# Kernel optimization log

Measured on AMD Instinct MI355X. Metric: run time of the kernel, lower is better.

## Reference

```python
import jax, jax.numpy as jnp
import numpy as np

B, DIN, D = 1000, 1024, 512
C, L = 1203, 77
N_INS, N_EX = 4, 5
K_SEL, K_TOP = 32, 5
HEADS, DH, MLP, NL = 8, 64, 2048, 4
TEMP = 50.0


def setup_inputs() -> dict:
    key = jax.random.key(0)
    ks = iter(jax.random.split(key, 64))

    def rn(shape, s=0.02):
        return jax.random.normal(next(ks), shape, dtype=jnp.float32) * s

    def layer_params(prefix):
        return {
            prefix + '_ln1_g': jnp.ones((NL, D)), prefix + '_ln1_b': jnp.zeros((NL, D)),
            prefix + '_qkv_w': rn((NL, D, 3 * D)), prefix + '_qkv_b': jnp.zeros((NL, 3 * D)),
            prefix + '_out_w': rn((NL, D, D)), prefix + '_out_b': jnp.zeros((NL, D)),
            prefix + '_ln2_g': jnp.ones((NL, D)), prefix + '_ln2_b': jnp.zeros((NL, D)),
            prefix + '_fc_w': rn((NL, D, MLP)), prefix + '_fc_b': jnp.zeros((NL, MLP)),
            prefix + '_pr_w': rn((NL, MLP, D)), prefix + '_pr_b': jnp.zeros((NL, D)),
        }

    zw = jax.random.normal(next(ks), (D, C + 1), dtype=jnp.float32)
    zw = zw / jnp.linalg.norm(zw, axis=0, keepdims=True)  # F.normalize(dim=0) as in __init__
    inp = {
        'x': jax.random.normal(next(ks), (B, DIN), dtype=jnp.float32),
        'linear_w': rn((DIN, D)), 'linear_b': jnp.zeros((D,)),
        'zs_weight': zw,
        'sample_w': rn((D, D)), 'sample_b': jnp.zeros((D,)),
        'ins_token': rn((N_INS, D), 0.1),
        'token_seq': rn((C, L, D), 0.1),
        'exemplar': rn((C, N_EX, D), 0.1),
        'eos_index': jax.random.randint(next(ks), (C,), 5, 60, dtype=jnp.int32),
    }
    inp.update(layer_params('agg'))
    inp['pos_emb'] = rn((L, D), 0.01)
    inp.update(layer_params('txt'))
    inp['lnf_g'] = jnp.ones((D,))
    inp['lnf_b'] = jnp.zeros((D,))
    inp['text_proj'] = rn((D, D))
    return inp


def layernorm(x, g, b, eps=1e-5):
    m = x.mean(-1, keepdims=True)
    v = x.var(-1, keepdims=True)
    return (x - m) * jax.lax.rsqrt(v + eps) * g + b


def quick_gelu(x):  # CLIP QuickGELU
    return x * jax.nn.sigmoid(1.702 * x)


def transformer(h, ln1g, ln1b, qkvw, qkvb, ow, ob, ln2g, ln2b, fcw, fcb, prw, prb, mask=None):
    # h: [N, S, D]; pre-LN residual attention blocks (CLIP style)
    Bn, S, _ = h.shape
    scale = np.float32(1.0 / np.sqrt(DH))
    for i in range(NL):
        a = layernorm(h, ln1g[i], ln1b[i])
        qkv = a @ qkvw[i] + qkvb[i]
        q, k, v = jnp.split(qkv, 3, axis=-1)
        q = q.reshape(Bn, S, HEADS, DH)
        k = k.reshape(Bn, S, HEADS, DH)
        v = v.reshape(Bn, S, HEADS, DH)
        s = jnp.einsum('bqhd,bkhd->bhqk', q, k) * scale
        if mask is not None:
            s = s + mask
        o = jnp.einsum('bhqk,bkhd->bqhd', jax.nn.softmax(s, axis=-1), v).reshape(Bn, S, D)
        h = h + o @ ow[i] + ob[i]
        m = layernorm(h, ln2g[i], ln2b[i])
        h = h + quick_gelu(m @ fcw[i] + fcb[i]) @ prw[i] + prb[i]
    return h


def inverse_sigmoid(x, eps=1e-5):
    x = jnp.clip(x, 0.0, 1.0)
    x1 = jnp.clip(x, eps, None)
    x2 = jnp.clip(1.0 - x, eps, None)
    return jnp.log(x1 / x2)


def reference(x, linear_w, linear_b, zs_weight, sample_w, sample_b, ins_token, token_seq,
              exemplar, eos_index,
              agg_ln1_g, agg_ln1_b, agg_qkv_w, agg_qkv_b, agg_out_w, agg_out_b,
              agg_ln2_g, agg_ln2_b, agg_fc_w, agg_fc_b, agg_pr_w, agg_pr_b,
              pos_emb, txt_ln1_g, txt_ln1_b, txt_qkv_w, txt_qkv_b, txt_out_w, txt_out_b,
              txt_ln2_g, txt_ln2_b, txt_fc_w, txt_fc_b, txt_pr_w, txt_pr_b,
              lnf_g, lnf_b, text_proj):
    # ---- base classifier ----
    h = x @ linear_w + linear_b                                        # [B, D]
    h = TEMP * h / jnp.linalg.norm(h, axis=1, keepdims=True)
    logits = h @ zs_weight                                             # [B, C+1]
    # ---- entropy-based proposal selection (eval path, k=32) ----
    p = jax.nn.sigmoid(logits)
    entropy = (-p * jax.nn.log_sigmoid(logits)).sum(-1)                # [B]
    _, select_index = jax.lax.top_k(entropy, K_SEL)                    # [32]
    sel_logits = logits[select_index]                                  # [32, C+1]
    _, topk_index = jax.lax.top_k(sel_logits[:, :-1], K_TOP)           # [32, 5]
    sampled_x = jax.lax.stop_gradient(h[select_index]) @ sample_w + sample_b  # [32, D]
    # ---- batched aggregator input (replaces per-proposal python loop) ----
    base = ins_token[None] + (sampled_x / TEMP)[:, None, :]            # [32, N_INS, D]
    base = jnp.broadcast_to(base[:, None], (K_SEL, K_TOP, N_INS, D))
    ex = exemplar[topk_index]                                          # [32, 5, N_EX, D]
    agg_in = jnp.concatenate([base, ex], axis=2).reshape(K_SEL * K_TOP, N_INS + N_EX, D)
    agg_out = transformer(agg_in, agg_ln1_g, agg_ln1_b, agg_qkv_w, agg_qkv_b, agg_out_w,
                          agg_out_b, agg_ln2_g, agg_ln2_b, agg_fc_w, agg_fc_b, agg_pr_w, agg_pr_b)
    ins_tokens = agg_out[:, :N_INS].reshape(K_SEL, K_TOP, N_INS, D)
    # ---- splice instance tokens into class prompts ----
    prompt = token_seq[topk_index]                                     # [32, 5, L, D]
    upd = jnp.concatenate([prompt[:, :, :2], ins_tokens, prompt[:, :, 2:L - N_INS]], axis=2)
    # ---- CLIP text encoder on updated prompts ----
    t = upd.reshape(K_SEL * K_TOP, L, D) + pos_emb
    causal = jnp.where(jnp.tril(jnp.ones((L, L), bool)), 0.0, -1e9).astype(jnp.float32)
    t = transformer(t, txt_ln1_g, txt_ln1_b, txt_qkv_w, txt_qkv_b, txt_out_w, txt_out_b,
                    txt_ln2_g, txt_ln2_b, txt_fc_w, txt_fc_b, txt_pr_w, txt_pr_b, mask=causal)
    t = layernorm(t, lnf_g, lnf_b)
    eos = (eos_index[topk_index] + 2 * N_INS).reshape(-1)              # [160]
    feats = t[jnp.arange(K_SEL * K_TOP), eos] @ text_proj              # [160, D]
    feats = feats / jnp.linalg.norm(feats, axis=-1, keepdims=True)
    rerank_logits = jnp.einsum('sd,skd->sk', sampled_x, feats.reshape(K_SEL, K_TOP, D))
    # ---- fuse + scatter back ----
    sel_det = jax.lax.stop_gradient(sel_logits)
    sel_topk = jnp.take_along_axis(sel_det, topk_index, axis=1)
    fused = jax.nn.sigmoid(sel_topk) ** 0.75 * jax.nn.sigmoid(rerank_logits) ** 0.25
    reranked = inverse_sigmoid(fused)
    rows = jnp.arange(K_SEL)[:, None]
    logits_clone = sel_det.at[rows, topk_index].set(reranked)
    logits_final = logits.at[select_index].set(logits_clone)
    return logits, rerank_logits, select_index, logits_final
```

## Files before the change

### kernel.cpp

```cpp
#include <hip/hip_runtime.h>
#include <math.h>

#define TID ((int)threadIdx.x)

constexpr int Bsz = 1000, DIN = 1024, Dm = 512, C1 = 1204, C0 = 1203, Ltok = 77;
constexpr int NINS = 4, NEX = 5, KSEL = 32, KTOP = 5, NHEAD = 8, DH = 64, MLPD = 2048, NL = 4, Pn = 160;
constexpr float TEMPc = 50.0f;

typedef __attribute__((ext_vector_type(8))) short short8;
typedef __attribute__((ext_vector_type(4))) float f32x4;
typedef __attribute__((address_space(1))) const void g1void;
typedef __attribute__((address_space(3))) void l3void;
#define GLOAD16(g, l) __builtin_amdgcn_global_load_lds((g1void*)(g), (l3void*)(l), 16, 0, 0)

__device__ __forceinline__ float sigf(float z) {
  return z >= 0.f ? 1.f / (1.f + expf(-z)) : expf(z) / (1.f + expf(z));
}

__device__ __forceinline__ float qgelu(float v) {
  return v * __fdividef(1.f, 1.f + __expf(-1.702f * v));
}

__device__ __forceinline__ unsigned short f2bfu(float f) {
  unsigned u = __builtin_bit_cast(unsigned, f);
  u += 0x7fffu + ((u >> 16) & 1u);
  return (unsigned short)(u >> 16);
}
__device__ __forceinline__ short f2bf(float f) { return (short)f2bfu(f); }

__global__ __launch_bounds__(256, 4) void bgemm_k(const short* __restrict__ A,
                                                  const short* __restrict__ Bt,
                                                  const float* __restrict__ bias,
                                                  float* __restrict__ Cf,
                                                  short* __restrict__ Cb,
                                                  float* __restrict__ Xres,
                                                  int M, int N, int K, int mode) {
  __shared__ short As[8192];
  __shared__ short Bs[8192];
  int nwg = gridDim.x * gridDim.y;
  int orig = blockIdx.y * gridDim.x + blockIdx.x;
  int xcd = orig & 7, lid = orig >> 3;
  int q = nwg >> 3, r = nwg & 7;
  int swz = (xcd < r ? xcd * (q + 1) : r * (q + 1) + (xcd - r) * q) + lid;
  int row0 = (swz / gridDim.x) * 128, col0 = (swz % gridDim.x) * 128;
  int lane = TID & 63;
  int w = TID >> 6;
  int wr = (TID >> 7) & 1, wc = (TID >> 6) & 1;
  int skb = (TID >> 4) & 3, si = TID & 15;
  f32x4 acc[4][4] = {};
  int nt = K >> 6;
  int kb = lane >> 4, i = lane & 15;
  for (int t = 0; t < nt; ++t) {
#pragma unroll
    for (int s = 0; s < 2; ++s) {
#pragma unroll
      for (int c = 0; c < 2; ++c) {
        int row = (c * 4 + w) * 16 + si;
        int k0 = (t << 6) + (s << 5) + skb * 8;
        GLOAD16(A + (size_t)(row0 + row) * K + k0, As + s * 4096 + (c * 256 + w * 64) * 8);
        GLOAD16(Bt + (size_t)(col0 + row) * K + k0, Bs + s * 4096 + (c * 256 + w * 64) * 8);
      }
    }
    __syncthreads();
#pragma unroll
    for (int s = 0; s < 2; ++s) {
      const short* Ab = As + s * 4096;
      const short* Bb = Bs + s * 4096;
      short8 af[4], bfr[4];
#pragma unroll
      for (int m = 0; m < 4; ++m)
        af[m] = *(const short8*)(Ab + ((((wr * 4 + m) * 4 + kb) * 16 + i) * 8));
#pragma unroll
      for (int n = 0; n < 4; ++n)
        bfr[n] = *(const short8*)(Bb + ((((wc * 4 + n) * 4 + kb) * 16 + i) * 8));
#pragma unroll
      for (int m = 0; m < 4; ++m)
#pragma unroll
        for (int n = 0; n < 4; ++n)
          acc[m][n] = __builtin_amdgcn_mfma_f32_16x16x32_bf16(bfr[n], af[m], acc[m][n], 0, 0, 0);
    }
    __syncthreads();
  }
  int li = lane & 15, lg = lane >> 4;
#pragma unroll
  for (int m = 0; m < 4; ++m) {
    int row = row0 + wr * 64 + m * 16 + li;
    if (row >= M) continue;
#pragma unroll
    for (int n = 0; n < 4; ++n) {
      int colb = col0 + wc * 64 + n * 16 + lg * 4;
      f32x4 v = acc[m][n];
      if (bias) {
        float4 bv = *(const float4*)(bias + colb);
        v[0] += bv.x; v[1] += bv.y; v[2] += bv.z; v[3] += bv.w;
      }
      size_t off = (size_t)row * N + colb;
      if (mode == 0) {
        *(float4*)(Cf + off) = make_float4(v[0], v[1], v[2], v[3]);
      } else if (mode == 1) {
        float4* p = (float4*)(Xres + off);
        float4 o = *p;
        o.x += v[0]; o.y += v[1]; o.z += v[2]; o.w += v[3];
        *p = o;
      } else {
        if (mode == 2) {
          v[0] = qgelu(v[0]); v[1] = qgelu(v[1]); v[2] = qgelu(v[2]); v[3] = qgelu(v[3]);
        }
        uint2 pk;
        pk.x = (unsigned)f2bfu(v[0]) | ((unsigned)f2bfu(v[1]) << 16);
        pk.y = (unsigned)f2bfu(v[2]) | ((unsigned)f2bfu(v[3]) << 16);
        *(uint2*)(Cb + off) = pk;
      }
    }
  }
}

__global__ __launch_bounds__(256, 4) void bgemm_sk_k(const short* __restrict__ A,
                                                     const short* __restrict__ Bt,
                                                     float* __restrict__ P,
                                                     int M, int N, int K, int KC) {
  __shared__ short As[8192];
  __shared__ short Bs[8192];
  int nwg = gridDim.x * gridDim.y;
  int orig = blockIdx.y * gridDim.x + blockIdx.x;
  int xcd = orig & 7, lid = orig >> 3;
  int q = nwg >> 3, r = nwg & 7;
  int swz = (xcd < r ? xcd * (q + 1) : r * (q + 1) + (xcd - r) * q) + lid;
  int row0 = (swz / gridDim.x) * 128, col0 = (swz % gridDim.x) * 128;
  int kbeg = blockIdx.z * KC;
  int lane = TID & 63;
  int w = TID >> 6;
  int wr = (TID >> 7) & 1, wc = (TID >> 6) & 1;
  int skb = (TID >> 4) & 3, si = TID & 15;
  f32x4 acc[4][4] = {};
  int nt = KC >> 6;
  int kb = lane >> 4, i = lane & 15;
  for (int t = 0; t < nt; ++t) {
#pragma unroll
    for (int s = 0; s < 2; ++s) {
#pragma unroll
      for (int c = 0; c < 2; ++c) {
        int row = (c * 4 + w) * 16 + si;
        int k0 = kbeg + (t << 6) + (s << 5) + skb * 8;
        GLOAD16(A + (size_t)(row0 + row) * K + k0, As + s * 4096 + (c * 256 + w * 64) * 8);
        GLOAD16(Bt + (size_t)(col0 + row) * K + k0, Bs + s * 4096 + (c * 256 + w * 64) * 8);
      }
    }
    __syncthreads();
#pragma unroll
    for (int s = 0; s < 2; ++s) {
      const short* Ab = As + s * 4096;
      const short* Bb = Bs + s * 4096;
      short8 af[4], bfr[4];
#pragma unroll
      for (int m = 0; m < 4; ++m)
        af[m] = *(const short8*)(Ab + ((((wr * 4 + m) * 4 + kb) * 16 + i) * 8));
#pragma unroll
      for (int n = 0; n < 4; ++n)
        bfr[n] = *(const short8*)(Bb + ((((wc * 4 + n) * 4 + kb) * 16 + i) * 8));
#pragma unroll
      for (int m = 0; m < 4; ++m)
#pragma unroll
        for (int n = 0; n < 4; ++n)
          acc[m][n] = __builtin_amdgcn_mfma_f32_16x16x32_bf16(bfr[n], af[m], acc[m][n], 0, 0, 0);
    }
    __syncthreads();
  }
  float* Pz = P + (size_t)blockIdx.z * M * N;
  int li = lane & 15, lg = lane >> 4;
#pragma unroll
  for (int m = 0; m < 4; ++m) {
    int row = row0 + wr * 64 + m * 16 + li;
    if (row >= M) continue;
#pragma unroll
    for (int n = 0; n < 4; ++n) {
      int colb = col0 + wc * 64 + n * 16 + lg * 4;
      *(float4*)(Pz + (size_t)row * N + colb) = make_float4(acc[m][n][0], acc[m][n][1], acc[m][n][2], acc[m][n][3]);
    }
  }
}

__global__ __launch_bounds__(256) void reduce_res_k(const float* __restrict__ P,
                                                    const float* __restrict__ bias,
                                                    float* __restrict__ Xres,
                                                    int MN, int N, int S) {
  int i = blockIdx.x * 256 + TID;
  if (i >= MN) return;
  float v = bias[i % N];
  for (int s = 0; s < S; ++s) v += P[(size_t)s * MN + i];
  Xres[i] += v;
}

__global__ __launch_bounds__(256) void wconv_k(const float* __restrict__ W,
                                               short* __restrict__ Wt, int K, int N) {
  int l = blockIdx.z;
  const float* Wl = W + (size_t)l * K * N;
  short* Wtl = Wt + (size_t)l * K * N;
  __shared__ float t[32][33];
  int n0 = blockIdx.x * 32, k0 = blockIdx.y * 32;
  int tx = TID & 31, ty = TID >> 5;
#pragma unroll
  for (int u = 0; u < 4; ++u)
    t[ty + u * 8][tx] = Wl[(size_t)(k0 + ty + u * 8) * N + n0 + tx];
  __syncthreads();
#pragma unroll
  for (int u = 0; u < 4; ++u)
    Wtl[(size_t)(n0 + ty + u * 8) * K + k0 + tx] = f2bf(t[tx][ty + u * 8]);
}

__global__ __launch_bounds__(256) void gemm32s_k(const float* __restrict__ A,
                                                 const float* __restrict__ W,
                                                 float* __restrict__ P,
                                                 int M, int N, int K, int KC) {
  __shared__ float As[64][17];
  __shared__ float Ws[16][65];
  int tx = TID & 15, ty = TID >> 4;
  int row0 = blockIdx.y * 64, col0 = blockIdx.x * 64;
  int kbeg = blockIdx.z * KC;
  int kend = kbeg + KC < K ? kbeg + KC : K;
  float acc[4][4] = {};
  for (int k0 = kbeg; k0 < kend; k0 += 16) {
    {
      int r = TID >> 2, c4 = (TID & 3) * 4;
      int gr = row0 + r;
#pragma unroll
      for (int u = 0; u < 4; ++u) {
        int gc = k0 + c4 + u;
        As[r][c4 + u] = (gr < M && gc < K) ? A[gr * K + gc] : 0.f;
      }
    }
    {
      int c = TID & 63;
      int gc = col0 + c;
#pragma unroll
      for (int u = 0; u < 4; ++u) {
        int rr = (TID >> 6) * 4 + u;
        int gk = k0 + rr;
        Ws[rr][c] = (gk < K && gc < N) ? W[gk * N + gc] : 0.f;
      }
    }
    __syncthreads();
#pragma unroll
    for (int kk = 0; kk < 16; ++kk) {
      float a[4], b[4];
#pragma unroll
      for (int i = 0; i < 4; ++i) a[i] = As[ty * 4 + i][kk];
#pragma unroll
      for (int j = 0; j < 4; ++j) b[j] = Ws[kk][tx * 4 + j];
#pragma unroll
      for (int i = 0; i < 4; ++i)
#pragma unroll
        for (int j = 0; j < 4; ++j) acc[i][j] += a[i] * b[j];
    }
    __syncthreads();
  }
  float* Ps = P + (size_t)blockIdx.z * M * N;
#pragma unroll
  for (int i = 0; i < 4; ++i) {
    int rrow = row0 + ty * 4 + i;
    if (rrow >= M) continue;
#pragma unroll
    for (int j = 0; j < 4; ++j) {
      int ccol = col0 + tx * 4 + j;
      if (ccol >= N) continue;
      Ps[(size_t)rrow * N + ccol] = acc[i][j];
    }
  }
}

__global__ __launch_bounds__(256) void reduce_k(const float* __restrict__ P,
                                                const float* __restrict__ bias,
                                                float* __restrict__ C,
                                                float* __restrict__ C2,
                                                int MN, int N, int S) {
  int i = blockIdx.x * 256 + TID;
  if (i >= MN) return;
  float v = 0.f;
  for (int s = 0; s < S; ++s) v += P[(size_t)s * MN + i];
  if (bias) v += bias[i % N];
  C[i] = v;
  if (C2) C2[i] = v;
}

__global__ __launch_bounds__(256) void rownorm_k(float* __restrict__ h) {
  int r = blockIdx.x;
  float* x = h + r * Dm;
  float v0 = x[TID], v1 = x[TID + 256];
  __shared__ float s1[256];
  s1[TID] = v0 * v0 + v1 * v1;
  __syncthreads();
  for (int s = 128; s; s >>= 1) { if (TID < s) s1[TID] += s1[TID + s]; __syncthreads(); }
  float sc = TEMPc / sqrtf(s1[0]);
  x[TID] = v0 * sc;
  x[TID + 256] = v1 * sc;
}

__global__ __launch_bounds__(256) void entropy_k(const float* __restrict__ logits,
                                                 double* __restrict__ ent) {
  int r = blockIdx.x;
  double acc = 0.0;
  for (int c = TID; c < C1; c += 256) {
    float z = logits[r * C1 + c];
    float ls = z >= 0.f ? -log1pf(expf(-z)) : z - log1pf(expf(z));
    float p = z >= 0.f ? 1.f / (1.f + expf(-z)) : expf(z) / (1.f + expf(z));
    acc += (double)(-p * ls);
  }
  __shared__ double sd[256];
  sd[TID] = acc;
  __syncthreads();
  for (int s = 128; s; s >>= 1) { if (TID < s) sd[TID] += sd[TID + s]; __syncthreads(); }
  if (TID == 0) ent[r] = sd[0];
}

__global__ __launch_bounds__(256) void top32_k(const double* __restrict__ ent,
                                               int* __restrict__ selidx,
                                               float* __restrict__ out2) {
  __shared__ double v[1000];
  __shared__ double wv[4];
  __shared__ int wi[4];
  for (int i = TID; i < 1000; i += 256) v[i] = ent[i];
  __syncthreads();
  int w = TID >> 6, lane = TID & 63;
  for (int r = 0; r < KSEL; ++r) {
    double bv = -1e300; int bi = 1 << 30;
    for (int i = TID; i < 1000; i += 256) {
      double x = v[i];
      if (x > bv || (x == bv && i < bi)) { bv = x; bi = i; }
    }
#pragma unroll
    for (int off = 32; off; off >>= 1) {
      double ov = __shfl_xor(bv, off, 64);
      int oi = __shfl_xor(bi, off, 64);
      if (ov > bv || (ov == bv && oi < bi)) { bv = ov; bi = oi; }
    }
    if (lane == 0) { wv[w] = bv; wi[w] = bi; }
    __syncthreads();
    if (TID == 0) {
      double fv = wv[0]; int fi = wi[0];
#pragma unroll
      for (int u = 1; u < 4; ++u)
        if (wv[u] > fv || (wv[u] == fv && wi[u] < fi)) { fv = wv[u]; fi = wi[u]; }
      selidx[r] = fi; out2[r] = (float)fi; v[fi] = -1e300;
    }
    __syncthreads();
  }
}

__global__ __launch_bounds__(256) void top5_k(const float* __restrict__ logits,
                                              const int* __restrict__ selidx,
                                              int* __restrict__ topk) {
  int s = blockIdx.x;
  int row = selidx[s];
  __shared__ float v[C0];
  __shared__ float wv[4];
  __shared__ int wi[4];
  for (int i = TID; i < C0; i += 256) v[i] = logits[row * C1 + i];
  __syncthreads();
  int w = TID >> 6, lane = TID & 63;
  for (int r = 0; r < KTOP; ++r) {
    float bv = -INFINITY; int bi = 1 << 30;
    for (int i = TID; i < C0; i += 256) {
      float x = v[i];
      if (x > bv || (x == bv && i < bi)) { bv = x; bi = i; }
    }
#pragma unroll
    for (int off = 32; off; off >>= 1) {
      float ov = __shfl_xor(bv, off, 64);
      int oi = __shfl_xor(bi, off, 64);
      if (ov > bv || (ov == bv && oi < bi)) { bv = ov; bi = oi; }
    }
    if (lane == 0) { wv[w] = bv; wi[w] = bi; }
    __syncthreads();
    if (TID == 0) {
      float fv = wv[0]; int fi = wi[0];
#pragma unroll
      for (int u = 1; u < 4; ++u)
        if (wv[u] > fv || (wv[u] == fv && wi[u] < fi)) { fv = wv[u]; fi = wi[u]; }
      topk[s * KTOP + r] = fi; v[fi] = -INFINITY;
    }
    __syncthreads();
  }
}

__global__ void eos_k(const int* __restrict__ eos_index, const int* __restrict__ topk,
                      int* __restrict__ eosl) {
  for (int p = TID; p < Pn; p += 256) eosl[p] = eos_index[topk[p]] + 2 * NINS;
}

__global__ void gather_h_k(const float* __restrict__ h, const int* __restrict__ selidx,
                           float* __restrict__ hsel) {
  int s = blockIdx.x;
  int row = selidx[s];
  for (int d = TID; d < Dm; d += 256) hsel[s * Dm + d] = h[row * Dm + d];
}

__global__ __launch_bounds__(256) void build_agg_k(const float* __restrict__ ins,
                                                   const float* __restrict__ sampled,
                                                   const float* __restrict__ ex,
                                                   const int* __restrict__ topk,
                                                   float* __restrict__ X) {
  int b = blockIdx.x;
  int p = b / 9, tok = b % 9;
  int s = p / KTOP;
#pragma unroll
  for (int u = 0; u < 2; ++u) {
    int d = TID + u * 256;
    float v;
    if (tok < NINS) v = ins[tok * Dm + d] + sampled[s * Dm + d] * (1.f / TEMPc);
    else {
      int cls = topk[p];
      v = ex[(cls * NEX + (tok - NINS)) * Dm + d];
    }
    X[b * Dm + d] = v;
  }
}

__global__ void save_ins_k(const float* __restrict__ X, float* __restrict__ insbuf) {
  int p = blockIdx.x;
  for (int i = TID; i < NINS * Dm; i += 256) insbuf[p * NINS * Dm + i] = X[p * 9 * Dm + i];
}

__global__ __launch_bounds__(256) void build_txt_k(const float* __restrict__ token_seq,
                                                   const float* __restrict__ insbuf,
                                                   const float* __restrict__ pos,
                                                   const int* __restrict__ topk,
                                                   float* __restrict__ X, int p0) {
  int b = blockIdx.x;
  int pl = b / Ltok, tok = b % Ltok;
  int p = p0 + pl;
  int cls = topk[p];
#pragma unroll
  for (int u = 0; u < 2; ++u) {
    int d = TID + u * 256;
    float v;
    if (tok < 2) v = token_seq[(cls * Ltok + tok) * Dm + d];
    else if (tok < 2 + NINS) v = insbuf[(p * NINS + (tok - 2)) * Dm + d];
    else v = token_seq[(cls * Ltok + (tok - NINS)) * Dm + d];
    X[b * Dm + d] = v + pos[tok * Dm + d];
  }
}

__global__ __launch_bounds__(256) void ln_k(const float* __restrict__ X,
                                            const float* __restrict__ g,
                                            const float* __restrict__ b,
                                            short* __restrict__ A) {
  int t = blockIdx.x;
  const float* x = X + t * Dm;
  float v0 = x[TID], v1 = x[TID + 256];
  __shared__ float s1[256], s2[256];
  s1[TID] = v0 + v1;
  s2[TID] = v0 * v0 + v1 * v1;
  __syncthreads();
  for (int s = 128; s; s >>= 1) {
    if (TID < s) { s1[TID] += s1[TID + s]; s2[TID] += s2[TID + s]; }
    __syncthreads();
  }
  float mean = s1[0] * (1.f / 512.f);
  float var = s2[0] * (1.f / 512.f) - mean * mean;
  float inv = rsqrtf(var + 1e-5f);
  A[t * Dm + TID] = f2bf((v0 - mean) * inv * g[TID] + b[TID]);
  A[t * Dm + TID + 256] = f2bf((v1 - mean) * inv * g[TID + 256] + b[TID + 256]);
}

__global__ __launch_bounds__(320) void attn_tx_k(const short* __restrict__ qkv,
                                                 short* __restrict__ O, int S) {
  __shared__ short Kf[5120];
  __shared__ short Vt[6144];
  __shared__ short Pf[5][1536];
  int p = blockIdx.x >> 3, h = blockIdx.x & 7;
  int base = p * S;
  for (int c = TID; c < 640; c += 320) {
    int i = c & 15, kb = (c >> 4) & 7, g = c >> 7;
    int j = g * 16 + i;
    short8 v = {};
    if (j < S) v = *(const short8*)(qkv + (size_t)(base + j) * 1536 + 512 + h * 64 + kb * 8);
    *(short8*)(Kf + c * 8) = v;
  }
  for (int c = TID; c < 640; c += 320) {
    int j = c >> 3;
    int d0 = (c & 7) * 8;
    short8 v = {};
    if (j < S) v = *(const short8*)(qkv + (size_t)(base + j) * 1536 + 1024 + h * 64 + d0);
    int kb = j >> 3, jj = j & 7;
#pragma unroll
    for (int u = 0; u < 8; ++u) {
      int d = d0 + u;
      Vt[(((d >> 4) * 12 + kb) * 16 + (d & 15)) * 8 + jj] = v[u];
    }
  }
  for (int c = TID; c < 128; c += 320) {
    int i = c & 15, kb = 10 + ((c >> 4) & 1), g = c >> 5;
    *(short8*)(Vt + ((g * 12 + kb) * 16 + i) * 8) = short8{};
  }
  __syncthreads();
  int w = TID >> 6, lane = TID & 63;
  int li = lane & 15, lg = lane >> 4;
  short8 aq[2];
#pragma unroll
  for (int ks = 0; ks < 2; ++ks)
    aq[ks] = *(const short8*)(qkv + (size_t)(base + w * 16 + li) * 1536 + h * 64 + ks * 32 + lg * 8);
  f32x4 accs[5] = {};
#pragma unroll
  for (int t = 0; t < 5; ++t)
#pragma unroll
    for (int ks = 0; ks < 2; ++ks) {
      short8 bk = *(const short8*)(Kf + ((t * 8 + ks * 4 + lg) * 16 + li) * 8);
      accs[t] = __builtin_amdgcn_mfma_f32_16x16x32_bf16(aq[ks], bk, accs[t], 0, 0, 0);
    }
  int rowg = w * 16 + lg * 4;
#pragma unroll
  for (int r = 0; r < 4; ++r) {
    int row = rowg + r;
    float v[5];
    float mx = -1e30f;
#pragma unroll
    for (int t = 0; t < 5; ++t) {
      int col = t * 16 + li;
      float x = accs[t][r] * 0.125f;
      bool ok = (col < S) && (col <= row);
      v[t] = ok ? x : -1e30f;
      mx = fmaxf(mx, v[t]);
    }
#pragma unroll
    for (int off = 1; off < 16; off <<= 1) mx = fmaxf(mx, __shfl_xor(mx, off, 64));
    float sum = 0.f;
#pragma unroll
    for (int t = 0; t < 5; ++t) {
      v[t] = (v[t] > -1e29f) ? __expf(v[t] - mx) : 0.f;
      sum += v[t];
    }
#pragma unroll
    for (int off = 1; off < 16; off <<= 1) sum += __shfl_xor(sum, off, 64);
    float inv = __fdividef(1.f, sum);
#pragma unroll
    for (int t = 0; t < 5; ++t) {
      int c = t * 16 + li;
      Pf[w][((c >> 3) * 16 + (row - w * 16)) * 8 + (c & 7)] = f2bf(v[t] * inv);
    }
  }
  for (int z = lane; z < 256; z += 64) {
    int kb = 10 + (z >> 7);
    int rem = z & 127;
    Pf[w][(kb * 16 + (rem >> 3)) * 8 + (rem & 7)] = 0;
  }
  f32x4 acco[4] = {};
#pragma unroll
  for (int s = 0; s < 3; ++s) {
    short8 ap = *(const short8*)(Pf[w] + ((s * 4 + lg) * 16 + li) * 8);
#pragma unroll
    for (int n = 0; n < 4; ++n) {
      short8 bv = *(const short8*)(Vt + ((n * 12 + s * 4 + lg) * 16 + li) * 8);
      acco[n] = __builtin_amdgcn_mfma_f32_16x16x32_bf16(ap, bv, acco[n], 0, 0, 0);
    }
  }
#pragma unroll
  for (int n = 0; n < 4; ++n)
#pragma unroll
    for (int r = 0; r < 4; ++r) {
      int row = rowg + r;
      if (row < S) O[(size_t)(base + row) * 512 + h * 64 + n * 16 + li] = f2bf(acco[n][r]);
    }
}

__global__ __launch_bounds__(256) void attn_k(const float* __restrict__ qkv,
                                              short* __restrict__ O, int S, int causal) {
  int blk = blockIdx.x;
  int p = blk >> 3, h = blk & 7;
  __shared__ float Qs[Ltok][68], Ks[Ltok][68], Vs[Ltok][68];
  __shared__ float ps[4][132];
  int base = p * S;
  for (int idx = TID; idx < S * 16; idx += 256) {
    int j = idx >> 4, c = idx & 15;
    const float4* q = (const float4*)(qkv + (size_t)(base + j) * 1536 + h * 64);
    const float4* k = (const float4*)(qkv + (size_t)(base + j) * 1536 + 512 + h * 64);
    const float4* v = (const float4*)(qkv + (size_t)(base + j) * 1536 + 1024 + h * 64);
    ((float4*)&Qs[j][0])[c] = q[c];
    ((float4*)&Ks[j][0])[c] = k[c];
    ((float4*)&Vs[j][0])[c] = v[c];
  }
  __syncthreads();
  int wave = TID >> 6, lane = TID & 63;
  bool val0 = lane < S, val1 = lane + 64 < S;
  int j0 = val0 ? lane : 0;
  int j1 = val1 ? lane + 64 : 0;
  const float4* k0p = (const float4*)&Ks[j0][0];
  const float4* k1p = (const float4*)&Ks[j1][0];
  for (int i = wave; i < S; i += 4) {
    const float4* q4 = (const float4*)&Qs[i][0];
    float a0 = 0.f, a1 = 0.f;
#pragma unroll
    for (int d4 = 0; d4 < 16; ++d4) {
      float4 qv = q4[d4], k0v = k0p[d4], k1v = k1p[d4];
      a0 += qv.x * k0v.x + qv.y * k0v.y + qv.z * k0v.z + qv.w * k0v.w;
      a1 += qv.x * k1v.x + qv.y * k1v.y + qv.z * k1v.z + qv.w * k1v.w;
    }
    float m0 = (val0 && (!causal || lane <= i)) ? a0 * 0.125f : -1e30f;
    float m1 = (val1 && (!causal || lane + 64 <= i)) ? a1 * 0.125f : -1e30f;
    float mx = fmaxf(m0, m1);
#pragma unroll
    for (int off = 32; off; off >>= 1) mx = fmaxf(mx, __shfl_xor(mx, off, 64));
    float e0 = expf(m0 - mx), e1 = expf(m1 - mx);
    float sum = e0 + e1;
#pragma unroll
    for (int off = 32; off; off >>= 1) sum += __shfl_xor(sum, off, 64);
    float inv = 1.f / sum;
    ps[wave][lane] = e0 * inv;
    ps[wave][lane + 64] = e1 * inv;
    float o = 0.f;
    for (int j = 0; j < S; ++j) o += ps[wave][j] * Vs[j][lane];
    O[(base + i) * Dm + h * 64 + lane] = f2bf(o);
  }
}

__global__ __launch_bounds__(256) void feats_k(const float* __restrict__ X,
                                               const int* __restrict__ eosl,
                                               const float* __restrict__ g,
                                               const float* __restrict__ bb,
                                               const float* __restrict__ proj,
                                               float* __restrict__ feats, int p0) {
  int pl = blockIdx.x;
  int p = p0 + pl;
  int e = eosl[p];
  const float* x = X + (size_t)(pl * Ltok + e) * Dm;
  __shared__ float row[Dm];
  __shared__ float s1[256], s2[256];
  float v0 = x[TID], v1 = x[TID + 256];
  s1[TID] = v0 + v1;
  s2[TID] = v0 * v0 + v1 * v1;
  __syncthreads();
  for (int s = 128; s; s >>= 1) {
    if (TID < s) { s1[TID] += s1[TID + s]; s2[TID] += s2[TID + s]; }
    __syncthreads();
  }
  float mean = s1[0] * (1.f / 512.f);
  float var = s2[0] * (1.f / 512.f) - mean * mean;
  float inv = rsqrtf(var + 1e-5f);
  row[TID] = (v0 - mean) * inv * g[TID] + bb[TID];
  row[TID + 256] = (v1 - mean) * inv * g[TID + 256] + bb[TID + 256];
  __syncthreads();
  float a0 = 0.f, a1 = 0.f;
  for (int d = 0; d < Dm; ++d) {
    float r = row[d];
    a0 += r * proj[d * Dm + TID];
    a1 += r * proj[d * Dm + TID + 256];
  }
  s1[TID] = a0 * a0 + a1 * a1;
  __syncthreads();
  for (int s = 128; s; s >>= 1) { if (TID < s) s1[TID] += s1[TID + s]; __syncthreads(); }
  float sc = 1.f / sqrtf(s1[0]);
  feats[p * Dm + TID] = a0 * sc;
  feats[p * Dm + TID + 256] = a1 * sc;
}

__global__ void rerank_k(const float* __restrict__ sampled, const float* __restrict__ feats,
                         const int* __restrict__ selidx, const int* __restrict__ topk,
                         const float* __restrict__ logits, float* __restrict__ out1,
                         float* __restrict__ out3) {
  int idx = blockIdx.x;
  int s = idx / KTOP;
  int lane = TID;
  float acc = 0.f;
  for (int d = lane; d < Dm; d += 64) acc += sampled[s * Dm + d] * feats[idx * Dm + d];
#pragma unroll
  for (int off = 32; off; off >>= 1) acc += __shfl_down(acc, off, 64);
  if (lane == 0) {
    out1[idx] = acc;
    int row = selidx[s];
    int cls = topk[idx];
    float sl = logits[row * C1 + cls];
    float a = sigf(sl), b = sigf(acc);
    float fused = powf(a, 0.75f) * powf(b, 0.25f);
    float xx = fminf(fmaxf(fused, 0.f), 1.f);
    float x1 = fmaxf(xx, 1e-5f);
    float x2 = fmaxf(1.f - xx, 1e-5f);
    out3[row * C1 + cls] = logf(x1 / x2);
  }
}

static inline size_t alup(size_t x) { return (x + 255) & ~(size_t)255; }

constexpr size_t WT_QKV = (size_t)NL * Dm * 3 * Dm;
constexpr size_t WT_OUT = (size_t)NL * Dm * Dm;
constexpr size_t WT_FC  = (size_t)NL * Dm * MLPD;
constexpr size_t WT_PR  = (size_t)NL * MLPD * Dm;
constexpr size_t WT_ALL = WT_QKV + WT_OUT + WT_FC + WT_PR;

static void plan_rows(int PC, size_t* rows_o, size_t* RP_o) {
  size_t rows = (size_t)PC * Ltok;
  if (rows < (size_t)(Pn * 9)) rows = Pn * 9;
  size_t RP = (rows + 127) & ~(size_t)127;
  *rows_o = rows; *RP_o = RP;
}

static size_t plan_bytes(int PC) {
  size_t rows, RP;
  plan_rows(PC, &rows, &RP);
  size_t tot = 0;
  tot += alup(Bsz * Dm * 4);
  tot += alup(Bsz * 8);
  tot += alup(KSEL * 4);
  tot += alup(Pn * 4);
  tot += alup(Pn * 4);
  tot += alup(KSEL * Dm * 4);
  tot += alup(KSEL * Dm * 4);
  tot += alup(Pn * NINS * Dm * 4);
  tot += alup(Pn * Dm * 4);
  tot += alup(rows * Dm * 4);
  tot += alup(RP * Dm * 2);
  tot += alup(RP * Dm * 2);
  tot += alup((size_t)(Pn * 9) * 3 * Dm * 4);
  tot += alup(RP * 3 * Dm * 2);
  tot += alup(RP * MLPD * 2);
  tot += 2 * alup(WT_ALL * 2);
  tot += alup((size_t)8 * Bsz * Dm * 4);
  tot += alup((size_t)4 * Bsz * C1 * 4);
  tot += alup((size_t)8 * KSEL * Dm * 4);
  tot += alup((size_t)4 * RP * Dm * 4);
  return tot;
}

extern "C" void kernel_launch(void* const* d_in, const int* in_sizes, int n_in,
                              void* d_out, int out_size, void* d_ws, size_t ws_size,
                              hipStream_t stream) {
  const float* x         = (const float*)d_in[0];
  const float* linear_w  = (const float*)d_in[1];
  const float* linear_b  = (const float*)d_in[2];
  const float* zs_w      = (const float*)d_in[3];
  const float* sample_w  = (const float*)d_in[4];
  const float* sample_b  = (const float*)d_in[5];
  const float* ins_token = (const float*)d_in[6];
  const float* token_seq = (const float*)d_in[7];
  const float* exemplar  = (const float*)d_in[8];
  const int*   eos_index = (const int*)d_in[9];
  const float* agg_ln1_g = (const float*)d_in[10];
  const float* agg_ln1_b = (const float*)d_in[11];
  const float* agg_qkv_w = (const float*)d_in[12];
  const float* agg_qkv_b = (const float*)d_in[13];
  const float* agg_out_w = (const float*)d_in[14];
  const float* agg_out_b = (const float*)d_in[15];
  const float* agg_ln2_g = (const float*)d_in[16];
  const float* agg_ln2_b = (const float*)d_in[17];
  const float* agg_fc_w  = (const float*)d_in[18];
  const float* agg_fc_b  = (const float*)d_in[19];
  const float* agg_pr_w  = (const float*)d_in[20];
  const float* agg_pr_b  = (const float*)d_in[21];
  const float* pos_emb   = (const float*)d_in[22];
  const float* txt_ln1_g = (const float*)d_in[23];
  const float* txt_ln1_b = (const float*)d_in[24];
  const float* txt_qkv_w = (const float*)d_in[25];
  const float* txt_qkv_b = (const float*)d_in[26];
  const float* txt_out_w = (const float*)d_in[27];
  const float* txt_out_b = (const float*)d_in[28];
  const float* txt_ln2_g = (const float*)d_in[29];
  const float* txt_ln2_b = (const float*)d_in[30];
  const float* txt_fc_w  = (const float*)d_in[31];
  const float* txt_fc_b  = (const float*)d_in[32];
  const float* txt_pr_w  = (const float*)d_in[33];
  const float* txt_pr_b  = (const float*)d_in[34];
  const float* lnf_g     = (const float*)d_in[35];
  const float* lnf_b     = (const float*)d_in[36];
  const float* text_proj = (const float*)d_in[37];

  float* out0 = (float*)d_out;
  float* out1 = out0 + Bsz * C1;
  float* out2 = out1 + KSEL * KTOP;
  float* out3 = out2 + KSEL;

  int PC = 20;
  const int cands[4] = {160, 80, 40, 20};
  for (int i = 0; i < 4; ++i)
    if (plan_bytes(cands[i]) <= ws_size) { PC = cands[i]; break; }
  int NC = Pn / PC;

  char* wp = (char*)d_ws;
  auto carve = [&](size_t bytes) -> void* { void* r = (void*)wp; wp += alup(bytes); return r; };
  size_t rows, RP;
  plan_rows(PC, &rows, &RP);

  float* h       = (float*)carve(Bsz * Dm * 4);
  double* ent    = (double*)carve(Bsz * 8);
  int* selidx    = (int*)carve(KSEL * 4);
  int* topk      = (int*)carve(Pn * 4);
  int* eosl      = (int*)carve(Pn * 4);
  float* hsel    = (float*)carve(KSEL * Dm * 4);
  float* sampled = (float*)carve(KSEL * Dm * 4);
  float* insbuf  = (float*)carve(Pn * NINS * Dm * 4);
  float* feats   = (float*)carve(Pn * Dm * 4);
  float* X       = (float*)carve(rows * Dm * 4);
  short* Abuf    = (short*)carve(RP * Dm * 2);
  short* Obuf    = (short*)carve(RP * Dm * 2);
  float* QKV     = (float*)carve((size_t)(Pn * 9) * 3 * Dm * 4);
  short* QKVb    = (short*)carve(RP * 3 * Dm * 2);
  short* Hb      = (short*)carve(RP * MLPD * 2);
  short* wtA     = (short*)carve(WT_ALL * 2);
  short* wtT     = (short*)carve(WT_ALL * 2);
  float* Plin    = (float*)carve((size_t)8 * Bsz * Dm * 4);
  float* Pzs     = (float*)carve((size_t)4 * Bsz * C1 * 4);
  float* Psmp    = (float*)carve((size_t)8 * KSEL * Dm * 4);
  float* Psk     = (float*)carve((size_t)4 * RP * Dm * 4);

  short* wtA_qkv = wtA;
  short* wtA_out = wtA_qkv + WT_QKV;
  short* wtA_fc  = wtA_out + WT_OUT;
  short* wtA_pr  = wtA_fc + WT_FC;
  short* wtT_qkv = wtT;
  short* wtT_out = wtT_qkv + WT_QKV;
  short* wtT_fc  = wtT_out + WT_OUT;
  short* wtT_pr  = wtT_fc + WT_FC;

  dim3 blk(256);
  auto wconv = [&](const float* W, short* Wt, int K, int N) {
    dim3 g(N / 32, K / 32, NL);
    wconv_k<<<g, blk, 0, stream>>>(W, Wt, K, N);
  };
  auto bgemm = [&](const short* A, const short* Wt, const float* bias, float* Cf, short* Cb,
                   float* Xres, int M, int N, int K, int mode) {
    dim3 g(N / 128, (M + 127) / 128);
    bgemm_k<<<g, blk, 0, stream>>>(A, Wt, bias, Cf, Cb, Xres, M, N, K, mode);
  };
  auto bgemm_res_sk = [&](const short* A, const short* Wt, const float* bias, float* Xres,
                          int M, int N, int K, int S) {
    dim3 g(N / 128, (M + 127) / 128, S);
    bgemm_sk_k<<<g, blk, 0, stream>>>(A, Wt, Psk, M, N, K, K / S);
    int MN = M * N;
    reduce_res_k<<<(MN + 255) / 256, blk, 0, stream>>>(Psk, bias, Xres, MN, N, S);
  };
  auto gemm32s = [&](const float* A, const float* W, float* P, int M, int N, int K, int S) {
    dim3 g((N + 63) / 64, (M + 63) / 64, S);
    gemm32s_k<<<g, blk, 0, stream>>>(A, W, P, M, N, K, K / S);
  };
  auto reduce = [&](const float* P, const float* bias, float* C, float* C2, int MN, int N, int S) {
    reduce_k<<<(MN + 255) / 256, blk, 0, stream>>>(P, bias, C, C2, MN, N, S);
  };

  wconv(agg_qkv_w, wtA_qkv, Dm, 3 * Dm);
  wconv(agg_out_w, wtA_out, Dm, Dm);
  wconv(agg_fc_w,  wtA_fc,  Dm, MLPD);
  wconv(agg_pr_w,  wtA_pr,  MLPD, Dm);
  wconv(txt_qkv_w, wtT_qkv, Dm, 3 * Dm);
  wconv(txt_out_w, wtT_out, Dm, Dm);
  wconv(txt_fc_w,  wtT_fc,  Dm, MLPD);
  wconv(txt_pr_w,  wtT_pr,  MLPD, Dm);

  gemm32s(x, linear_w, Plin, Bsz, Dm, DIN, 8);
  reduce(Plin, linear_b, h, nullptr, Bsz * Dm, Dm, 8);
  rownorm_k<<<Bsz, blk, 0, stream>>>(h);
  gemm32s(h, zs_w, Pzs, Bsz, C1, Dm, 4);
  reduce(Pzs, nullptr, out0, out3, Bsz * C1, C1, 4);
  entropy_k<<<Bsz, blk, 0, stream>>>(out0, ent);
  top32_k<<<1, blk, 0, stream>>>(ent, selidx, out2);
  top5_k<<<KSEL, blk, 0, stream>>>(out0, selidx, topk);
  eos_k<<<1, blk, 0, stream>>>(eos_index, topk, eosl);
  gather_h_k<<<KSEL, blk, 0, stream>>>(h, selidx, hsel);
  gemm32s(hsel, sample_w, Psmp, KSEL, Dm, Dm, 8);
  reduce(Psmp, sample_b, sampled, nullptr, KSEL * Dm, Dm, 8);

  build_agg_k<<<Pn * 9, blk, 0, stream>>>(ins_token, sampled, exemplar, topk, X);
  {
    int M = Pn * 9;
    for (int i = 0; i < NL; ++i) {
      ln_k<<<M, blk, 0, stream>>>(X, agg_ln1_g + i * Dm, agg_ln1_b + i * Dm, Abuf);
      bgemm(Abuf, wtA_qkv + (size_t)i * Dm * 3 * Dm, agg_qkv_b + i * 3 * Dm, QKV, nullptr, nullptr, M, 3 * Dm, Dm, 0);
      attn_k<<<Pn * NHEAD, blk, 0, stream>>>(QKV, Obuf, 9, 0);
      bgemm_res_sk(Obuf, wtA_out + (size_t)i * Dm * Dm, agg_out_b + i * Dm, X, M, Dm, Dm, 2);
      ln_k<<<M, blk, 0, stream>>>(X, agg_ln2_g + i * Dm, agg_ln2_b + i * Dm, Abuf);
      bgemm(Abuf, wtA_fc + (size_t)i * Dm * MLPD, agg_fc_b + i * MLPD, nullptr, Hb, nullptr, M, MLPD, Dm, 2);
      bgemm_res_sk(Hb, wtA_pr + (size_t)i * MLPD * Dm, agg_pr_b + i * Dm, X, M, Dm, MLPD, 4);
    }
  }
  save_ins_k<<<Pn, blk, 0, stream>>>(X, insbuf);

  for (int c = 0; c < NC; ++c) {
    int p0 = c * PC;
    int M = PC * Ltok;
    build_txt_k<<<PC * Ltok, blk, 0, stream>>>(token_seq, insbuf, pos_emb, topk, X, p0);
    for (int i = 0; i < NL; ++i) {
      ln_k<<<M, blk, 0, stream>>>(X, txt_ln1_g + i * Dm, txt_ln1_b + i * Dm, Abuf);
      bgemm(Abuf, wtT_qkv + (size_t)i * Dm * 3 * Dm, txt_qkv_b + i * 3 * Dm, nullptr, QKVb, nullptr, M, 3 * Dm, Dm, 3);
      attn_tx_k<<<dim3(PC * NHEAD), dim3(320), 0, stream>>>(QKVb, Obuf, Ltok);
      bgemm_res_sk(Obuf, wtT_out + (size_t)i * Dm * Dm, txt_out_b + i * Dm, X, M, Dm, Dm, 2);
      ln_k<<<M, blk, 0, stream>>>(X, txt_ln2_g + i * Dm, txt_ln2_b + i * Dm, Abuf);
      bgemm(Abuf, wtT_fc + (size_t)i * Dm * MLPD, txt_fc_b + i * MLPD, nullptr, Hb, nullptr, M, MLPD, Dm, 2);
      bgemm_res_sk(Hb, wtT_pr + (size_t)i * MLPD * Dm, txt_pr_b + i * Dm, X, M, Dm, MLPD, 4);
    }
    feats_k<<<PC, blk, 0, stream>>>(X, eosl, lnf_g, lnf_b, text_proj, feats, p0);
  }

  rerank_k<<<Pn, dim3(64), 0, stream>>>(sampled, feats, selidx, topk, out0, out1, out3);
}
```

Baseline: 1.990 ms.

## Drop split-K residual GEMMs and add 256-row tall GEMM tile for wide outputs

Replaces the split-K out-projection and MLP-down GEMMs plus their separate reduction kernel with the regular bf16 GEMM, which adds into the residual directly in its epilogue. This removes the partial-sum buffer traffic and an extra launch per call. It also adds a 512-thread kernel with 256x128 tiles for large-M, wide-N GEMMs (QKV and FC) to raise A/B reuse, padding row allocation to 256. The trade-off is fewer workgroups for the N=512 GEMMs, with no K-split to fill the GPU, and higher LDS use per block in the tall kernel.

```diff
diff --git a/kernel.cpp b/kernel.cpp
--- a/kernel.cpp
+++ b/kernel.cpp
@@ -27,6 +27,30 @@
   return (unsigned short)(u >> 16);
 }
 __device__ __forceinline__ short f2bf(float f) { return (short)f2bfu(f); }
+
+__device__ __forceinline__ void epi_store(f32x4 v, const float* bias, int colb, size_t off,
+                                          int mode, float* Cf, short* Cb, float* Xres) {
+  if (bias) {
+    float4 bv = *(const float4*)(bias + colb);
+    v[0] += bv.x; v[1] += bv.y; v[2] += bv.z; v[3] += bv.w;
+  }
+  if (mode == 0) {
+    *(float4*)(Cf + off) = make_float4(v[0], v[1], v[2], v[3]);
+  } else if (mode == 1) {
+    float4* p = (float4*)(Xres + off);
+    float4 o = *p;
+    o.x += v[0]; o.y += v[1]; o.z += v[2]; o.w += v[3];
+    *p = o;
+  } else {
+    if (mode == 2) {
+      v[0] = qgelu(v[0]); v[1] = qgelu(v[1]); v[2] = qgelu(v[2]); v[3] = qgelu(v[3]);
+    }
+    uint2 pk;
+    pk.x = (unsigned)f2bfu(v[0]) | ((unsigned)f2bfu(v[1]) << 16);
+    pk.y = (unsigned)f2bfu(v[2]) | ((unsigned)f2bfu(v[3]) << 16);
+    *(uint2*)(Cb + off) = pk;
+  }
+}
 
 __global__ __launch_bounds__(256, 4) void bgemm_k(const short* __restrict__ A,
                                                   const short* __restrict__ Bt,
@@ -89,67 +113,51 @@
 #pragma unroll
     for (int n = 0; n < 4; ++n) {
       int colb = col0 + wc * 64 + n * 16 + lg * 4;
-      f32x4 v = acc[m][n];
-      if (bias) {
-        float4 bv = *(const float4*)(bias + colb);
-        v[0] += bv.x; v[1] += bv.y; v[2] += bv.z; v[3] += bv.w;
-      }
-      size_t off = (size_t)row * N + colb;
-      if (mode == 0) {
-        *(float4*)(Cf + off) = make_float4(v[0], v[1], v[2], v[3]);
-      } else if (mode == 1) {
-        float4* p = (float4*)(Xres + off);
-        float4 o = *p;
-        o.x += v[0]; o.y += v[1]; o.z += v[2]; o.w += v[3];
-        *p = o;
-      } else {
-        if (mode == 2) {
-          v[0] = qgelu(v[0]); v[1] = qgelu(v[1]); v[2] = qgelu(v[2]); v[3] = qgelu(v[3]);
-        }
-        uint2 pk;
-        pk.x = (unsigned)f2bfu(v[0]) | ((unsigned)f2bfu(v[1]) << 16);
-        pk.y = (unsigned)f2bfu(v[2]) | ((unsigned)f2bfu(v[3]) << 16);
-        *(uint2*)(Cb + off) = pk;
-      }
-    }
-  }
-}
-
-__global__ __launch_bounds__(256, 4) void bgemm_sk_k(const short* __restrict__ A,
-                                                     const short* __restrict__ Bt,
-                                                     float* __restrict__ P,
-                                                     int M, int N, int K, int KC) {
-  __shared__ short As[8192];
+      epi_store(acc[m][n], bias, colb, (size_t)row * N + colb, mode, Cf, Cb, Xres);
+    }
+  }
+}
+
+__global__ __launch_bounds__(512, 4) void bgemm_tall_k(const short* __restrict__ A,
+                                                       const short* __restrict__ Bt,
+                                                       const float* __restrict__ bias,
+                                                       float* __restrict__ Cf,
+                                                       short* __restrict__ Cb,
+                                                       float* __restrict__ Xres,
+                                                       int M, int N, int K, int mode) {
+  __shared__ short As[16384];
   __shared__ short Bs[8192];
   int nwg = gridDim.x * gridDim.y;
   int orig = blockIdx.y * gridDim.x + blockIdx.x;
   int xcd = orig & 7, lid = orig >> 3;
   int q = nwg >> 3, r = nwg & 7;
   int swz = (xcd < r ? xcd * (q + 1) : r * (q + 1) + (xcd - r) * q) + lid;
-  int row0 = (swz / gridDim.x) * 128, col0 = (swz % gridDim.x) * 128;
-  int kbeg = blockIdx.z * KC;
+  int row0 = (swz / gridDim.x) * 256, col0 = (swz % gridDim.x) * 128;
   int lane = TID & 63;
   int w = TID >> 6;
-  int wr = (TID >> 7) & 1, wc = (TID >> 6) & 1;
-  int skb = (TID >> 4) & 3, si = TID & 15;
+  int wr = w >> 1, wc = w & 1;
   f32x4 acc[4][4] = {};
-  int nt = KC >> 6;
+  int nt = K >> 6;
   int kb = lane >> 4, i = lane & 15;
+  int sg0 = TID >> 6, skb = (TID >> 4) & 3, si = TID & 15;
   for (int t = 0; t < nt; ++t) {
 #pragma unroll
     for (int s = 0; s < 2; ++s) {
-#pragma unroll
-      for (int c = 0; c < 2; ++c) {
-        int row = (c * 4 + w) * 16 + si;
-        int k0 = kbeg + (t << 6) + (s << 5) + skb * 8;
-        GLOAD16(A + (size_t)(row0 + row) * K + k0, As + s * 4096 + (c * 256 + w * 64) * 8);
-        GLOAD16(Bt + (size_t)(col0 + row) * K + k0, Bs + s * 4096 + (c * 256 + w * 64) * 8);
+      int k0 = (t << 6) + (s << 5) + skb * 8;
+#pragma unroll
+      for (int c0 = 0; c0 < 2; ++c0) {
+        int row = (c0 * 8 + sg0) * 16 + si;
+        GLOAD16(A + (size_t)(row0 + row) * K + k0, As + s * 8192 + (c0 * 512 + TID) * 8);
       }
+      {
+        int row = sg0 * 16 + si;
+        GLOAD16(Bt + (size_t)(col0 + row) * K + k0, Bs + s * 4096 + TID * 8);
+      }
     }
     __syncthreads();
 #pragma unroll
     for (int s = 0; s < 2; ++s) {
-      const short* Ab = As + s * 4096;
+      const short* Ab = As + s * 8192;
       const short* Bb = Bs + s * 4096;
       short8 af[4], bfr[4];
 #pragma unroll
@@ -166,7 +174,6 @@
     }
     __syncthreads();
   }
-  float* Pz = P + (size_t)blockIdx.z * M * N;
   int li = lane & 15, lg = lane >> 4;
 #pragma unroll
   for (int m = 0; m < 4; ++m) {
@@ -175,20 +182,9 @@
 #pragma unroll
     for (int n = 0; n < 4; ++n) {
       int colb = col0 + wc * 64 + n * 16 + lg * 4;
-      *(float4*)(Pz + (size_t)row * N + colb) = make_float4(acc[m][n][0], acc[m][n][1], acc[m][n][2], acc[m][n][3]);
-    }
-  }
-}
-
-__global__ __launch_bounds__(256) void reduce_res_k(const float* __restrict__ P,
-                                                    const float* __restrict__ bias,
-                                                    float* __restrict__ Xres,
-                                                    int MN, int N, int S) {
-  int i = blockIdx.x * 256 + TID;
-  if (i >= MN) return;
-  float v = bias[i % N];
-  for (int s = 0; s < S; ++s) v += P[(size_t)s * MN + i];
-  Xres[i] += v;
+      epi_store(acc[m][n], bias, colb, (size_t)row * N + colb, mode, Cf, Cb, Xres);
+    }
+  }
 }
 
 __global__ __launch_bounds__(256) void wconv_k(const float* __restrict__ W,
@@ -688,7 +684,7 @@
 static void plan_rows(int PC, size_t* rows_o, size_t* RP_o) {
   size_t rows = (size_t)PC * Ltok;
   if (rows < (size_t)(Pn * 9)) rows = Pn * 9;
-  size_t RP = (rows + 127) & ~(size_t)127;
+  size_t RP = (rows + 255) & ~(size_t)255;
   *rows_o = rows; *RP_o = RP;
 }
 
@@ -715,7 +711,6 @@
   tot += alup((size_t)8 * Bsz * Dm * 4);
   tot += alup((size_t)4 * Bsz * C1 * 4);
   tot += alup((size_t)8 * KSEL * Dm * 4);
-  tot += alup((size_t)4 * RP * Dm * 4);
   return tot;
 }
 
@@ -797,7 +792,6 @@
   float* Plin    = (float*)carve((size_t)8 * Bsz * Dm * 4);
   float* Pzs     = (float*)carve((size_t)4 * Bsz * C1 * 4);
   float* Psmp    = (float*)carve((size_t)8 * KSEL * Dm * 4);
-  float* Psk     = (float*)carve((size_t)4 * RP * Dm * 4);
 
   short* wtA_qkv = wtA;
   short* wtA_out = wtA_qkv + WT_QKV;
@@ -815,15 +809,13 @@
   };
   auto bgemm = [&](const short* A, const short* Wt, const float* bias, float* Cf, short* Cb,
                    float* Xres, int M, int N, int K, int mode) {
-    dim3 g(N / 128, (M + 127) / 128);
-    bgemm_k<<<g, blk, 0, stream>>>(A, Wt, bias, Cf, Cb, Xres, M, N, K, mode);
-  };
-  auto bgemm_res_sk = [&](const short* A, const short* Wt, const float* bias, float* Xres,
-                          int M, int N, int K, int S) {
-    dim3 g(N / 128, (M + 127) / 128, S);
-    bgemm_sk_k<<<g, blk, 0, stream>>>(A, Wt, Psk, M, N, K, K / S);
-    int MN = M * N;
-    reduce_res_k<<<(MN + 255) / 256, blk, 0, stream>>>(Psk, bias, Xres, MN, N, S);
+    if (M >= 2048 && N >= 1536) {
+      dim3 g(N / 128, (M + 255) / 256);
+      bgemm_tall_k<<<g, dim3(512), 0, stream>>>(A, Wt, bias, Cf, Cb, Xres, M, N, K, mode);
+    } else {
+      dim3 g(N / 128, (M + 127) / 128);
+      bgemm_k<<<g, blk, 0, stream>>>(A, Wt, bias, Cf, Cb, Xres, M, N, K, mode);
+    }
   };
   auto gemm32s = [&](const float* A, const float* W, float* P, int M, int N, int K, int S) {
     dim3 g((N + 63) / 64, (M + 63) / 64, S);
@@ -862,10 +854,10 @@
       ln_k<<<M, blk, 0, stream>>>(X, agg_ln1_g + i * Dm, agg_ln1_b + i * Dm, Abuf);
       bgemm(Abuf, wtA_qkv + (size_t)i * Dm * 3 * Dm, agg_qkv_b + i * 3 * Dm, QKV, nullptr, nullptr, M, 3 * Dm, Dm, 0);
       attn_k<<<Pn * NHEAD, blk, 0, stream>>>(QKV, Obuf, 9, 0);
-      bgemm_res_sk(Obuf, wtA_out + (size_t)i * Dm * Dm, agg_out_b + i * Dm, X, M, Dm, Dm, 2);
+      bgemm(Obuf, wtA_out + (size_t)i * Dm * Dm, agg_out_b + i * Dm, nullptr, nullptr, X, M, Dm, Dm, 1);
       ln_k<<<M, blk, 0, stream>>>(X, agg_ln2_g + i * Dm, agg_ln2_b + i * Dm, Abuf);
       bgemm(Abuf, wtA_fc + (size_t)i * Dm * MLPD, agg_fc_b + i * MLPD, nullptr, Hb, nullptr, M, MLPD, Dm, 2);
-      bgemm_res_sk(Hb, wtA_pr + (size_t)i * MLPD * Dm, agg_pr_b + i * Dm, X, M, Dm, MLPD, 4);
+      bgemm(Hb, wtA_pr + (size_t)i * MLPD * Dm, agg_pr_b + i * Dm, nullptr, nullptr, X, M, Dm, MLPD, 1);
     }
   }
   save_ins_k<<<Pn, blk, 0, stream>>>(X, insbuf);
@@ -878,10 +870,10 @@
       ln_k<<<M, blk, 0, stream>>>(X, txt_ln1_g + i * Dm, txt_ln1_b + i * Dm, Abuf);
       bgemm(Abuf, wtT_qkv + (size_t)i * Dm * 3 * Dm, txt_qkv_b + i * 3 * Dm, nullptr, QKVb, nullptr, M, 3 * Dm, Dm, 3);
       attn_tx_k<<<dim3(PC * NHEAD), dim3(320), 0, stream>>>(QKVb, Obuf, Ltok);
-      bgemm_res_sk(Obuf, wtT_out + (size_t)i * Dm * Dm, txt_out_b + i * Dm, X, M, Dm, Dm, 2);
+      bgemm(Obuf, wtT_out + (size_t)i * Dm * Dm, txt_out_b + i * Dm, nullptr, nullptr, X, M, Dm, Dm, 1);
       ln_k<<<M, blk, 0, stream>>>(X, txt_ln2_g + i * Dm, txt_ln2_b + i * Dm, Abuf);
       bgemm(Abuf, wtT_fc + (size_t)i * Dm * MLPD, txt_fc_b + i * MLPD, nullptr, Hb, nullptr, M, MLPD, Dm, 2);
-      bgemm_res_sk(Hb, wtT_pr + (size_t)i * MLPD * Dm, txt_pr_b + i * Dm, X, M, Dm, MLPD, 4);
+      bgemm(Hb, wtT_pr + (size_t)i * MLPD * Dm, txt_pr_b + i * Dm, nullptr, nullptr, X, M, Dm, MLPD, 1);
     }
     feats_k<<<PC, blk, 0, stream>>>(X, eosl, lnf_g, lnf_b, text_proj, feats, p0);
   }
```

After: 1.972 ms. Within noise of the previous version (-0.9%).
